# Performance work log

Measured on AMD Instinct MI355X. Metric: run time of the kernel, lower is better.

Reference implementation:

```python
import jax, jax.numpy as jnp
import numpy as np

N = 10000   # num_nodes
F = 64      # latent_dim
U = 128     # num_units
B = 8       # batch
K = 2       # gcn_step
E = 160000  # edges (avg degree 16)
M = 2 * K + 1  # num_matrices = len(supports)*gcn_step + 1


def setup_inputs() -> dict:
    rng = np.random.default_rng(0)
    rows = rng.integers(0, N, E).astype(np.int32)
    cols = rng.integers(0, N, E).astype(np.int32)
    vals = (rng.random(E).astype(np.float32) + 0.1)
    # random-walk normalization D^{-1} A, per the original utils.calculate_random_walk_matrix
    deg_out = np.zeros(N, np.float32); np.add.at(deg_out, rows, vals)
    deg_in = np.zeros(N, np.float32); np.add.at(deg_in, cols, vals)
    # support1 = (D_out^{-1} A)^T : out[c] += vals/d_out[r] * x[r]  -> dst=cols, src=rows
    w1 = vals / np.maximum(deg_out[rows], 1e-8)
    # support2 = (D_in^{-1} A^T)^T : out[r] += vals/d_in[c] * x[c]  -> dst=rows, src=cols
    w2 = vals / np.maximum(deg_in[cols], 1e-8)

    key = jax.random.key(0)
    ks = jax.random.split(key, 4)

    def xavier(k, shape):
        std = (2.0 / (shape[0] + shape[1])) ** 0.5
        return jax.random.normal(k, shape, jnp.float32) * std

    return {
        'y': jax.random.normal(ks[0], (B, N * F), jnp.float32),
        'W_lat': xavier(ks[1], (M * F, F)),
        'b_lat': jnp.ones((F,), jnp.float32),   # bias_start=1.0, shared (keyed by length)
        'W_units': xavier(ks[2], (M * F, U)),
        'b_units': jnp.zeros((U,), jnp.float32),
        'W_final': xavier(ks[3], (M * U, F)),
        'sup1_w': jnp.asarray(w1),
        'sup2_w': jnp.asarray(w2),
        'edge_rows': jnp.asarray(rows),
        'edge_cols': jnp.asarray(cols),
    }


def _spmm(dst, src, w, x):
    # sparse matmul S @ x with S given as COO edge list; x: (N, Fin, B)
    return jax.ops.segment_sum(w[:, None, None] * x[src], dst, num_segments=N)


def _gconv(x, supports, W, b):
    # x: (B, N, Fin) -> (B, N*Fout); Chebyshev diffusion convolution
    Bsz, n, fin = x.shape
    x0 = jnp.transpose(x, (1, 2, 0))  # (N, Fin, B)
    xs = [x0]
    for dst, src, w in supports:
        xk_2 = x0
        x1 = _spmm(dst, src, w, x0)
        xs.append(x1)
        for _ in range(2, K + 1):
            x2 = 2.0 * _spmm(dst, src, w, x1) - xk_2
            xs.append(x2)
            xk_2, x1 = x1, x2
    X = jnp.stack(xs, axis=-1)                       # (N, Fin, B, M)
    X = jnp.transpose(X, (2, 0, 1, 3)).reshape(Bsz * n, fin * len(xs))  # feature-major, matrix-minor
    out = X @ W + b
    return out.reshape(Bsz, n * W.shape[1])


def reference(y, W_lat, b_lat, W_units, b_units, W_final, sup1_w, sup2_w, edge_rows, edge_cols):
    supports = [(edge_cols, edge_rows, sup1_w), (edge_rows, edge_cols, sup2_w)]
    x = y.reshape(B, N, F)
    # theta gate (bias_start=1.0 via shared b_lat)
    theta = jax.nn.sigmoid(_gconv(x, supports, W_lat, b_lat))
    # ode_func_net: gen_layers=1 hidden gconv + final gconv (final bias is shared b_lat!)
    c = jnp.tanh(_gconv(x, supports, W_units, b_units)).reshape(B, N, U)
    c = jnp.tanh(_gconv(c, supports, W_final, b_lat))
    return -theta * c
```

## Files before the change

kernel.cpp:

```cpp
#include <hip/hip_runtime.h>

#define N_NODES 10000
#define NEDGE 160000
#define NB 80000
#define EPAD (NEDGE + 8 * N_NODES)

typedef unsigned int u32;
typedef unsigned short u16;
typedef __attribute__((ext_vector_type(8))) short short8;
typedef __attribute__((ext_vector_type(4))) float float4v;

__device__ __forceinline__ u16 f2bf(float f) {
    u32 u = __float_as_uint(f);
    return (u16)((u + 0x7fffu + ((u >> 16) & 1u)) >> 16);
}
__device__ __forceinline__ float lo16(u32 u) { return __uint_as_float(u << 16); }
__device__ __forceinline__ float hi16(u32 u) { return __uint_as_float(u & 0xffff0000u); }
__device__ __forceinline__ u32 pack2(float a, float b) {
    return (u32)f2bf(a) | (((u32)f2bf(b)) << 16);
}
__device__ __forceinline__ float fast_tanh(float v) {
    return 1.f - 2.f / (__expf(2.f * v) + 1.f);
}

static const size_t SLAB = (size_t)NB * 64;

__global__ __launch_bounds__(256) void prepcount_kernel(
    const float2* __restrict__ y, u32* __restrict__ X0,
    const float* __restrict__ W_lat, const float* __restrict__ W_units,
    u16* __restrict__ bpk12, const float* __restrict__ W_final, u16* __restrict__ bpkP,
    const int* __restrict__ rows, const int* __restrict__ cols, int* __restrict__ cnt) {
    int b = blockIdx.x, t = threadIdx.x;
    if (b < 10000) {
        int idx = b * 256 + t;
        int fh = idx & 31;
        int rb = idx >> 5;
        int bb = rb & 7;
        int n = rb >> 3;
        float2 v = y[((size_t)bb * N_NODES + n) * 32 + fh];
        X0[idx] = pack2(v.x, v.y);
    } else if (b < 10240) {
        int idx = (b - 10000) * 256 + t;
        int j = idx & 7;
        int lane = (idx >> 3) & 63;
        int rest = idx >> 9;
        int ct = rest % 12;
        int ks = rest / 12;
        int k = ks * 32 + (lane >> 4) * 8 + j;
        int col = ct * 16 + (lane & 15);
        int wrow = (k % 64) * 5 + (k / 64);
        float v = (col < 64) ? W_lat[wrow * 64 + col] : W_units[wrow * 128 + (col - 64)];
        bpk12[idx] = f2bf(v);
    } else if (b < 10400) {
        int idx = (b - 10240) * 256 + t;
        int j8 = idx & 7;
        int lane = (idx >> 3) & 63;
        int rest = idx >> 9;
        int ct = rest % 20;
        int ks = rest / 20;
        int k = ks * 32 + (lane >> 4) * 8 + j8;
        int col = ct * 16 + (lane & 15);
        int slot = col >> 6, j = col & 63;
        float v;
        if (slot == 0)
            v = W_final[(k * 5 + 0) * 64 + j] - W_final[(k * 5 + 2) * 64 + j] -
                W_final[(k * 5 + 4) * 64 + j];
        else
            v = W_final[(k * 5 + slot) * 64 + j];
        bpkP[idx] = f2bf(v);
    } else {
        int e = (b - 10400) * 256 + t;
        atomicAdd(&cnt[cols[e]], 1);
        atomicAdd(&cnt[N_NODES + rows[e]], 1);
    }
}

__global__ void blocksum_kernel(const int* __restrict__ cnt, int* __restrict__ bsums) {
    __shared__ int red[4];
    int arr = blockIdx.x / 40;
    int c = blockIdx.x % 40;
    int idx = c * 256 + threadIdx.x;
    int v = (idx < N_NODES) ? ((cnt[arr * N_NODES + idx] + 7) & ~7) : 0;
#pragma unroll
    for (int off = 32; off; off >>= 1) v += __shfl_down(v, off, 64);
    int wv = threadIdx.x >> 6, ln = threadIdx.x & 63;
    if (ln == 0) red[wv] = v;
    __syncthreads();
    if (threadIdx.x == 0) bsums[blockIdx.x] = red[0] + red[1] + red[2] + red[3];
}

__global__ void scanapply_kernel(int* __restrict__ cnt, const int* __restrict__ bsums,
                                 int* __restrict__ rowptr1, int* __restrict__ rowptr2) {
    __shared__ int lds[256];
    int arr = blockIdx.x / 40;
    int c = blockIdx.x % 40;
    int base = 0;
    for (int i = 0; i < c; i++) base += bsums[arr * 40 + i];
    int idx = c * 256 + threadIdx.x;
    bool ok = idx < N_NODES;
    int v = ok ? ((cnt[arr * N_NODES + idx] + 7) & ~7) : 0;
    int t = threadIdx.x;
    lds[t] = v;
    __syncthreads();
    for (int off = 1; off < 256; off <<= 1) {
        int add = (t >= off) ? lds[t - off] : 0;
        __syncthreads();
        lds[t] += add;
        __syncthreads();
    }
    int excl = lds[t] - v + base;
    if (ok) {
        int* rp = arr ? rowptr2 : rowptr1;
        rp[idx] = excl;
        cnt[arr * N_NODES + idx] = excl;
    }
    if (c == 39 && t == 255) {
        (arr ? rowptr2 : rowptr1)[N_NODES] = base + lds[255];
    }
}

__global__ void scatter_kernel(const int* __restrict__ rows, const int* __restrict__ cols,
                               const float* __restrict__ w1, const float* __restrict__ w2,
                               int* __restrict__ cur1, int* __restrict__ cur2,
                               int2* __restrict__ edges1, int2* __restrict__ edges2) {
    int e = blockIdx.x * 256 + threadIdx.x;
    if (e < NEDGE) {
        int r = rows[e], c = cols[e];
        int p1 = atomicAdd(&cur1[c], 1);
        edges1[p1] = make_int2(r, __float_as_int(w1[e]));
        int p2 = atomicAdd(&cur2[r], 1);
        edges2[p2] = make_int2(c, __float_as_int(w2[e]));
    }
}

__device__ __forceinline__ void gacc(float* acc, float w, uint4 u) {
    acc[0] += w * lo16(u.x); acc[1] += w * hi16(u.x);
    acc[2] += w * lo16(u.y); acc[3] += w * hi16(u.y);
    acc[4] += w * lo16(u.z); acc[5] += w * hi16(u.z);
    acc[6] += w * lo16(u.w); acc[7] += w * hi16(u.w);
}

__device__ __forceinline__ void gather_sliced(const u32* __restrict__ Xin,
                                              const int* __restrict__ rp,
                                              const int2* __restrict__ eg,
                                              int row, bool valid, int su, int l,
                                              float* acc) {
    int e = 0, e1 = 0;
    if (valid) {
        e = rp[row] + l;
        e1 = rp[row + 1];
    }
    while (__ballot(e < e1)) {
        int2 me = make_int2(0, 0);
        if (e < e1) me = eg[e];
#pragma unroll
        for (int j = 0; j < 8; j++) {
            int s = __shfl(me.x, j, 8);
            float w = __int_as_float(__shfl(me.y, j, 8));
            uint4 u = *(const uint4*)(Xin + (size_t)s * 256 + su + l * 4);
            gacc(acc, w, u);
        }
        e += 8;
    }
}

__global__ __launch_bounds__(256) void spmm2_kernel(
    const u32* __restrict__ XinA, const u32* __restrict__ XprevA, u32* __restrict__ XoutA,
    const u32* __restrict__ XinB, const u32* __restrict__ XprevB, u32* __restrict__ XoutB,
    const int* __restrict__ rowptr1, const int2* __restrict__ edges1,
    const int* __restrict__ rowptr2, const int2* __restrict__ edges2,
    float alpha, float beta) {
    int t = threadIdx.x;
    int lane = t & 63;
    int g = lane >> 3, l = lane & 7;
    int slice = blockIdx.x & 7;
    int chunk = blockIdx.x >> 3;
    int su = slice * 32;
    int v = chunk * 32 + (t >> 6) * 8 + g;
    bool hB = v >= N_NODES;
    int n = hB ? v - N_NODES : v;
    const u32* Xin = hB ? XinB : XinA;
    const u32* Xprev = hB ? XprevB : XprevA;
    u32* Xout = hB ? XoutB : XoutA;
    const int* rp = hB ? rowptr2 : rowptr1;
    const int2* eg = hB ? edges2 : edges1;

    float acc[8] = {0.f, 0.f, 0.f, 0.f, 0.f, 0.f, 0.f, 0.f};
    gather_sliced(Xin, rp, eg, n, true, su, l, acc);

    size_t o = (size_t)n * 256 + su + l * 4;
    if (beta != 0.f) {
        uint4 p = *(const uint4*)(Xprev + o);
        acc[0] = alpha * acc[0] + beta * lo16(p.x); acc[1] = alpha * acc[1] + beta * hi16(p.x);
        acc[2] = alpha * acc[2] + beta * lo16(p.y); acc[3] = alpha * acc[3] + beta * hi16(p.y);
        acc[4] = alpha * acc[4] + beta * lo16(p.z); acc[5] = alpha * acc[5] + beta * hi16(p.z);
        acc[6] = alpha * acc[6] + beta * lo16(p.w); acc[7] = alpha * acc[7] + beta * hi16(p.w);
    } else {
#pragma unroll
        for (int i = 0; i < 8; i++) acc[i] *= alpha;
    }
    uint4 r;
    r.x = pack2(acc[0], acc[1]);
    r.y = pack2(acc[2], acc[3]);
    r.z = pack2(acc[4], acc[5]);
    r.w = pack2(acc[6], acc[7]);
    *(uint4*)(Xout + o) = r;
}

__global__ __launch_bounds__(256) void spmm_final_kernel(
    const u32* __restrict__ T1, const u32* __restrict__ T2,
    const u32* __restrict__ Q, const u32* __restrict__ theta,
    const int* __restrict__ rowptr1, const int2* __restrict__ edges1,
    const int* __restrict__ rowptr2, const int2* __restrict__ edges2,
    float* __restrict__ outF) {
    int t = threadIdx.x;
    int lane = t & 63;
    int g = lane >> 3, l = lane & 7;
    int slice = blockIdx.x & 7;
    int chunk = blockIdx.x >> 3;
    int su = slice * 32;
    int n = chunk * 32 + (t >> 6) * 8 + g;
    bool valid = n < N_NODES;

    float acc[8] = {0.f, 0.f, 0.f, 0.f, 0.f, 0.f, 0.f, 0.f};
    gather_sliced(T1, rowptr1, edges1, n, valid, su, l, acc);
    gather_sliced(T2, rowptr2, edges2, n, valid, su, l, acc);
    if (!valid) return;

    size_t o = (size_t)n * 256 + su + l * 4;
    uint4 q = *(const uint4*)(Q + o);
    uint4 th = *(const uint4*)(theta + o);
    float res[8];
    res[0] = -lo16(th.x) * fast_tanh(lo16(q.x) + acc[0]);
    res[1] = -hi16(th.x) * fast_tanh(hi16(q.x) + acc[1]);
    res[2] = -lo16(th.y) * fast_tanh(lo16(q.y) + acc[2]);
    res[3] = -hi16(th.y) * fast_tanh(hi16(q.y) + acc[3]);
    res[4] = -lo16(th.z) * fast_tanh(lo16(q.z) + acc[4]);
    res[5] = -hi16(th.z) * fast_tanh(hi16(q.z) + acc[5]);
    res[6] = -lo16(th.w) * fast_tanh(lo16(q.w) + acc[6]);
    res[7] = -hi16(th.w) * fast_tanh(hi16(q.w) + acc[7]);
    float* dst = outF + (size_t)slice * (N_NODES * 64) + (size_t)n * 64 + l * 8;
    *(float4*)(dst) = make_float4(res[0], res[1], res[2], res[3]);
    *(float4*)(dst + 4) = make_float4(res[4], res[5], res[6], res[7]);
}

struct Slabs { const u16* p[5]; };

template <int FIN, int NM, int NOUT, int NSPLIT, int MODE>
__global__ __launch_bounds__(512) void gemm_kernel(
    Slabs A, const u16* __restrict__ Bp, const float* __restrict__ bias1,
    const float* __restrict__ bias2, u16* __restrict__ O1, u16* __restrict__ O2) {
    constexpr int K = NM * FIN;
    constexpr int KS = K / 32;
    constexpr int CTT = NOUT / 16;
    constexpr int CT = CTT / NSPLIT;
    __shared__ u16 Blds[KS * CT * 64 * 8];

    int t = threadIdx.x;
    int lane = t & 63;
    int wave = t >> 6;
    int rowBase = (blockIdx.x / NSPLIT) * 128 + wave * 16;
    int ctBase = (blockIdx.x % NSPLIT) * CT;
    int mrow = lane & 15;
    int kq = lane >> 4;

    for (int idx = t; idx < KS * CT * 64; idx += 512) {
        int bl = idx & 63;
        int ct = (idx >> 6) % CT;
        int ks = idx / (64 * CT);
        *(uint4*)(Blds + (size_t)idx * 8) =
            *(const uint4*)(Bp + ((size_t)(ks * CTT + ctBase + ct) * 64 + bl) * 8);
    }
    __syncthreads();

    float4v acc[CT];
#pragma unroll
    for (int c = 0; c < CT; c++) acc[c] = (float4v){0.f, 0.f, 0.f, 0.f};

#pragma unroll
    for (int ks = 0; ks < KS; ks++) {
        int k = ks * 32 + kq * 8;
        int m = k / FIN;
        int koff = k % FIN;
        short8 a = *(const short8*)(A.p[m] + (size_t)(rowBase + mrow) * FIN + koff);
#pragma unroll
        for (int ct = 0; ct < CT; ct++) {
            short8 b = *(const short8*)(Blds + ((size_t)(ks * CT + ct) * 64 + lane) * 8);
            acc[ct] = __builtin_amdgcn_mfma_f32_16x16x32_bf16(a, b, acc[ct], 0, 0, 0);
        }
    }

    int rowq = rowBase + kq * 4;
#pragma unroll
    for (int ct = 0; ct < CT; ct++) {
        int col = (ctBase + ct) * 16 + mrow;
        float bsv;
        if (MODE == 0) bsv = (col < 64) ? bias1[col] : 0.f;
        else bsv = (col < 64) ? bias1[col] : bias2[col - 64];
#pragma unroll
        for (int i = 0; i < 4; i++) {
            float v = acc[ct][i] + bsv;
            int r = rowq + i;
            if (MODE == 0) {
                O1[(size_t)(col >> 6) * SLAB + (size_t)r * 64 + (col & 63)] = f2bf(v);
            } else {
                if (col < 64) {
                    v = 1.f / (1.f + __expf(-v));
                    O1[(size_t)r * 64 + col] = f2bf(v);
                } else {
                    O2[(size_t)r * 128 + (col - 64)] = f2bf(fast_tanh(v));
                }
            }
        }
    }
}

extern "C" void kernel_launch(void* const* d_in, const int* in_sizes, int n_in,
                              void* d_out, int out_size, void* d_ws, size_t ws_size,
                              hipStream_t stream) {
    const float2* y    = (const float2*)d_in[0];
    const float* W_lat = (const float*)d_in[1];
    const float* b_lat = (const float*)d_in[2];
    const float* W_units = (const float*)d_in[3];
    const float* b_units = (const float*)d_in[4];
    const float* W_final = (const float*)d_in[5];
    const float* sup1w = (const float*)d_in[6];
    const float* sup2w = (const float*)d_in[7];
    const int* rows    = (const int*)d_in[8];
    const int* cols    = (const int*)d_in[9];
    float* out = (float*)d_out;

    char* ws = (char*)d_ws;
    size_t off = 0;
    auto alloc = [&](size_t bytes) -> void* {
        void* p = ws + off;
        off += (bytes + 511) & ~(size_t)511;
        return p;
    };
    int* rowptr1 = (int*)alloc((N_NODES + 1) * 4);
    int* rowptr2 = (int*)alloc((N_NODES + 1) * 4);
    int* cnt = (int*)alloc((size_t)2 * N_NODES * 4);
    int* bsums = (int*)alloc(80 * 4);
    int2* edges1 = (int2*)alloc((size_t)EPAD * 8);
    int2* edges2 = (int2*)alloc((size_t)EPAD * 8);
    u16* bpk12 = (u16*)alloc((size_t)61440 * 2);
    u16* bpkP = (u16*)alloc((size_t)40960 * 2);
    u16* theta = (u16*)alloc((size_t)NB * 64 * 2);
    u16* S = (u16*)alloc((size_t)5 * NB * 64 * 2);
    u16* H0 = (u16*)alloc((size_t)NB * 128 * 2);
    u16* T1 = (u16*)alloc((size_t)NB * 64 * 2);
    u16* T2 = (u16*)alloc((size_t)NB * 64 * 2);

    hipMemsetAsync(cnt, 0, (size_t)2 * N_NODES * 4, stream);
    hipMemsetAsync(edges1, 0, (size_t)EPAD * 8, stream);
    hipMemsetAsync(edges2, 0, (size_t)EPAD * 8, stream);
    prepcount_kernel<<<11025, 256, 0, stream>>>(y, (u32*)S, W_lat, W_units, bpk12,
                                                W_final, bpkP, rows, cols, cnt);
    blocksum_kernel<<<80, 256, 0, stream>>>(cnt, bsums);
    scanapply_kernel<<<80, 256, 0, stream>>>(cnt, bsums, rowptr1, rowptr2);
    scatter_kernel<<<625, 256, 0, stream>>>(rows, cols, sup1w, sup2w,
                                            cnt, cnt + N_NODES, edges1, edges2);

    const u32* S0 = (const u32*)S;
    u32* X1 = (u32*)(S + 1 * SLAB);
    u32* X2 = (u32*)(S + 2 * SLAB);
    u32* X3 = (u32*)(S + 3 * SLAB);
    u32* X4 = (u32*)(S + 4 * SLAB);
    spmm2_kernel<<<5000, 256, 0, stream>>>(S0, nullptr, X1, S0, nullptr, X3,
                                           rowptr1, edges1, rowptr2, edges2, 1.f, 0.f);
    spmm2_kernel<<<5000, 256, 0, stream>>>(X1, S0, X2, X3, S0, X4,
                                           rowptr1, edges1, rowptr2, edges2, 2.f, -1.f);

    Slabs SX;
    for (int m = 0; m < 5; m++) SX.p[m] = S + (size_t)m * SLAB;
    gemm_kernel<64, 5, 192, 2, 1><<<1250, 512, 0, stream>>>(SX, bpk12, b_lat, b_units, theta, H0);

    Slabs SH;
    SH.p[0] = H0;
    gemm_kernel<128, 1, 320, 2, 0><<<1250, 512, 0, stream>>>(SH, bpkP, b_lat, nullptr, S, nullptr);

    const u32* Q  = (const u32*)(S + 0 * SLAB);
    const u32* P1 = (const u32*)(S + 1 * SLAB);
    const u32* P2 = (const u32*)(S + 2 * SLAB);
    const u32* P3 = (const u32*)(S + 3 * SLAB);
    const u32* P4 = (const u32*)(S + 4 * SLAB);
    spmm2_kernel<<<5000, 256, 0, stream>>>(P2, P1, (u32*)T1, P4, P3, (u32*)T2,
                                           rowptr1, edges1, rowptr2, edges2, 2.f, 1.f);
    spmm_final_kernel<<<2504, 256, 0, stream>>>((const u32*)T1, (const u32*)T2, Q,
                                                (const u32*)theta,
                                                rowptr1, edges1, rowptr2, edges2, out);
}
```

Baseline: 311.5 us.

## Remap GEMM blocks per batch slice and swap MFMA operands for vectorized stores

Result: slower. 334.9 us (+7.5%).

```diff
diff --git a/kernel.cpp b/kernel.cpp
--- a/kernel.cpp
+++ b/kernel.cpp
@@ -247,7 +247,7 @@
 struct Slabs { const u16* p[5]; };
 
 template <int FIN, int NM, int NOUT, int NSPLIT, int MODE>
-__global__ __launch_bounds__(512) void gemm_kernel(
+__global__ __launch_bounds__(320) void gemm_kernel(
     Slabs A, const u16* __restrict__ Bp, const float* __restrict__ bias1,
     const float* __restrict__ bias2, u16* __restrict__ O1, u16* __restrict__ O2) {
     constexpr int K = NM * FIN;
@@ -259,12 +259,16 @@
     int t = threadIdx.x;
     int lane = t & 63;
     int wave = t >> 6;
-    int rowBase = (blockIdx.x / NSPLIT) * 128 + wave * 16;
-    int ctBase = (blockIdx.x % NSPLIT) * CT;
+    int slice = blockIdx.x & 7;
+    int rest = blockIdx.x >> 3;
+    int nodeG = rest / NSPLIT;
+    int half = rest % NSPLIT;
+    int ctBase = half * CT;
     int mrow = lane & 15;
     int kq = lane >> 4;
-
-    for (int idx = t; idx < KS * CT * 64; idx += 512) {
+    int node0 = nodeG * 80 + wave * 16;
+
+    for (int idx = t; idx < KS * CT * 64; idx += 320) {
         int bl = idx & 63;
         int ct = (idx >> 6) % CT;
         int ks = idx / (64 * CT);
@@ -277,39 +281,47 @@
 #pragma unroll
     for (int c = 0; c < CT; c++) acc[c] = (float4v){0.f, 0.f, 0.f, 0.f};
 
+    size_t r = (size_t)(node0 + mrow) * 8 + slice;
 #pragma unroll
     for (int ks = 0; ks < KS; ks++) {
         int k = ks * 32 + kq * 8;
         int m = k / FIN;
         int koff = k % FIN;
-        short8 a = *(const short8*)(A.p[m] + (size_t)(rowBase + mrow) * FIN + koff);
+        short8 a = *(const short8*)(A.p[m] + r * FIN + koff);
 #pragma unroll
         for (int ct = 0; ct < CT; ct++) {
             short8 b = *(const short8*)(Blds + ((size_t)(ks * CT + ct) * 64 + lane) * 8);
-            acc[ct] = __builtin_amdgcn_mfma_f32_16x16x32_bf16(a, b, acc[ct], 0, 0, 0);
+            acc[ct] = __builtin_amdgcn_mfma_f32_16x16x32_bf16(b, a, acc[ct], 0, 0, 0);
         }
     }
 
-    int rowq = rowBase + kq * 4;
 #pragma unroll
     for (int ct = 0; ct < CT; ct++) {
-        int col = (ctBase + ct) * 16 + mrow;
-        float bsv;
-        if (MODE == 0) bsv = (col < 64) ? bias1[col] : 0.f;
-        else bsv = (col < 64) ? bias1[col] : bias2[col - 64];
-#pragma unroll
-        for (int i = 0; i < 4; i++) {
-            float v = acc[ct][i] + bsv;
-            int r = rowq + i;
-            if (MODE == 0) {
-                O1[(size_t)(col >> 6) * SLAB + (size_t)r * 64 + (col & 63)] = f2bf(v);
+        int col0 = (ctBase + ct) * 16 + kq * 4;
+        float v[4];
+#pragma unroll
+        for (int i = 0; i < 4; i++) v[i] = acc[ct][i];
+        if (MODE == 0) {
+            if (col0 < 64) {
+#pragma unroll
+                for (int i = 0; i < 4; i++) v[i] += bias1[col0 + i];
+            }
+            uint2 w = make_uint2(pack2(v[0], v[1]), pack2(v[2], v[3]));
+            u16* dst = O1 + (size_t)(col0 >> 6) * SLAB + r * 64 + (col0 & 63);
+            *(uint2*)dst = w;
+        } else {
+            if (col0 < 64) {
+#pragma unroll
+                for (int i = 0; i < 4; i++)
+                    v[i] = 1.f / (1.f + __expf(-(v[i] + bias1[col0 + i])));
+                uint2 w = make_uint2(pack2(v[0], v[1]), pack2(v[2], v[3]));
+                *(uint2*)(O1 + r * 64 + col0) = w;
             } else {
-                if (col < 64) {
-                    v = 1.f / (1.f + __expf(-v));
-                    O1[(size_t)r * 64 + col] = f2bf(v);
-                } else {
-                    O2[(size_t)r * 128 + (col - 64)] = f2bf(fast_tanh(v));
-                }
+#pragma unroll
+                for (int i = 0; i < 4; i++)
+                    v[i] = fast_tanh(v[i] + bias2[col0 - 64 + i]);
+                uint2 w = make_uint2(pack2(v[0], v[1]), pack2(v[2], v[3]));
+                *(uint2*)(O2 + r * 128 + (col0 - 64)) = w;
             }
         }
     }
@@ -373,11 +385,11 @@
 
     Slabs SX;
     for (int m = 0; m < 5; m++) SX.p[m] = S + (size_t)m * SLAB;
-    gemm_kernel<64, 5, 192, 2, 1><<<1250, 512, 0, stream>>>(SX, bpk12, b_lat, b_units, theta, H0);
+    gemm_kernel<64, 5, 192, 2, 1><<<2000, 320, 0, stream>>>(SX, bpk12, b_lat, b_units, theta, H0);
 
     Slabs SH;
     SH.p[0] = H0;
-    gemm_kernel<128, 1, 320, 2, 0><<<1250, 512, 0, stream>>>(SH, bpkP, b_lat, nullptr, S, nullptr);
+    gemm_kernel<128, 1, 320, 2, 0><<<2000, 320, 0, stream>>>(SH, bpkP, b_lat, nullptr, S, nullptr);
 
     const u32* Q  = (const u32*)(S + 0 * SLAB);
     const u32* P1 = (const u32*)(S + 1 * SLAB);
```
